# Optimization experiments

Hardware: AMD Instinct MI355X
Metric: run time of the kernel (lower is better)

Reference implementation:

```python
import jax, jax.numpy as jnp
import numpy as np

B, N, D, H, L, C = 64, 64, 64, 256, 64, 2


def setup_inputs() -> dict:
    key = jax.random.key(0)
    ks = iter(jax.random.split(key, 40))

    def p(*shape):
        return (jax.random.normal(next(ks), shape, jnp.float32) / np.sqrt(shape[0])).astype(jnp.float32)

    inp = {
        "x": jax.random.normal(next(ks), (B, N, D), jnp.float32),
        "adj": jax.random.uniform(next(ks), (B, N, N), jnp.float32),
        "condition": jax.random.normal(next(ks), (B, C), jnp.float32),
        # GraphConv layers
        "gc1_W": p(D, H), "gc1_b": jnp.zeros((H,)),
        "gc2_W": p(H, H), "gc2_b": jnp.zeros((H,)),
        "gc3mu_W": p(H, L), "gc3mu_b": jnp.zeros((L,)),
        "gc3lv_W": p(H, L), "gc3lv_b": jnp.zeros((L,)),
        # condition encoder
        "ce_W1": p(C, H), "ce_b1": jnp.zeros((H,)),
        "ce_W2": p(H, H), "ce_b2": jnp.zeros((H,)),
        # decoder
        "dec_W1": p(L + H, H), "dec_b1": jnp.zeros((H,)),
        "dec_W2": p(H, H), "dec_b2": jnp.zeros((H,)),
        "dec_W3": p(H, D), "dec_b3": jnp.zeros((D,)),
        # atom type predictor
        "at_W1": p(D, H), "at_b1": jnp.zeros((H,)),
        "at_W2": p(H, 8), "at_b2": jnp.zeros((8,)),
        # bond predictor
        "bp_W1": p(2 * D + H, H), "bp_b1": jnp.zeros((H,)),
        "bp_W2": p(H, H), "bp_b2": jnp.zeros((H,)),
        "bp_W3": p(H, 4), "bp_b3": jnp.zeros((4,)),
        # rule encoder
        "re_W1": p(D, H), "re_b1": jnp.zeros((H,)),
        "re_W2": p(H, 4), "re_b2": jnp.zeros((4,)),
    }
    return inp


def reference(x, adj, condition,
              gc1_W, gc1_b, gc2_W, gc2_b, gc3mu_W, gc3mu_b, gc3lv_W, gc3lv_b,
              ce_W1, ce_b1, ce_W2, ce_b2,
              dec_W1, dec_b1, dec_W2, dec_b2, dec_W3, dec_b3,
              at_W1, at_b1, at_W2, at_b2,
              bp_W1, bp_b1, bp_W2, bp_b2, bp_W3, bp_b3,
              re_W1, re_b1, re_W2, re_b2):
    relu = jax.nn.relu

    def gc(h, W, b):  # batched GraphConv: adj @ h then linear
        return jnp.einsum('bij,bjd->bid', adj, h) @ W + b

    # encode
    h = relu(gc(x, gc1_W, gc1_b))
    h = relu(gc(h, gc2_W, gc2_b))
    mu = gc(h, gc3mu_W, gc3mu_b)        # [B,N,L]
    logvar = gc(h, gc3lv_W, gc3lv_b)    # [B,N,L]
    z = mu  # eval-mode reparameterize (deterministic)

    # decode: condition encoding broadcast over nodes
    cond = relu(condition @ ce_W1 + ce_b1) @ ce_W2 + ce_b2  # [B,H]
    dec_in = jnp.concatenate([z, jnp.broadcast_to(cond[:, None, :], (z.shape[0], z.shape[1], cond.shape[-1]))], axis=-1)
    f = relu(dec_in @ dec_W1 + dec_b1)
    f = relu(f @ dec_W2 + dec_b2)
    features = jax.nn.sigmoid(f @ dec_W3 + dec_b3)  # [B,N,D]

    type_probs = jax.nn.softmax(relu(features @ at_W1 + at_b1) @ at_W2 + at_b2, axis=-1)  # [B,N,8]
    valence = jax.nn.sigmoid(relu(features @ re_W1 + re_b1) @ re_W2 + re_b2) * 4.0        # [B,N,4]
    atom_features = features * jnp.mean(type_probs, axis=-1, keepdims=True)               # [B,N,D]

    # dense pairwise bond probabilities (vectorized version of the per-pair MLP)
    b, n, d = atom_features.shape
    af_i = jnp.broadcast_to(atom_features[:, :, None, :], (b, n, n, d))
    af_j = jnp.broadcast_to(atom_features[:, None, :, :], (b, n, n, d))
    cnd = jnp.broadcast_to(cond[:, None, None, :], (b, n, n, cond.shape[-1]))
    pair = jnp.concatenate([af_i, af_j, cnd], axis=-1)  # [B,N,N,2D+H]
    g = relu(pair @ bp_W1 + bp_b1)
    g = relu(g @ bp_W2 + bp_b2)
    bond_probs = jax.nn.softmax(g @ bp_W3 + bp_b3, axis=-1)  # [B,N,N,4]

    return (atom_features, bond_probs, valence, mu, logvar)
```

## Files before the change

kernel.cpp:

```cpp
#include <hip/hip_runtime.h>

typedef short short8 __attribute__((ext_vector_type(8)));
typedef float f32x4 __attribute__((ext_vector_type(4)));
typedef unsigned short u16;
typedef unsigned int u32;

__device__ __forceinline__ u16 f2bf(float f) {
  union { float f; u32 u; } x; x.f = f;
  u32 u = x.u;
  u32 r = (u + 0x7FFFu + ((u >> 16) & 1u)) >> 16;
  return (u16)r;
}

__device__ __forceinline__ u32 cvtpk(float lo, float hi) {
  u32 r;
  asm("v_cvt_pk_bf16_f32 %0, %1, %2" : "=v"(r) : "v"(lo), "v"(hi));
  return r;
}

#define OW2T   0
#define OW3TX  65536
#define ODW1A  69632
#define ODW2   86016
#define ODW3   151552
#define OBPA   167936
#define OBPB   184320
#define OREW1  200704
#define OREW2  217088
#define OWMU   221184
#define OWLV   237568

__global__ void __launch_bounds__(512) k_pg(
    const float* __restrict__ cnd, const float* __restrict__ ceW1,
    const float* __restrict__ ceb1, const float* __restrict__ ceW2,
    const float* __restrict__ ceb2, const float* __restrict__ bpW1,
    const float* __restrict__ bpb1, const float* __restrict__ dW1,
    const float* __restrict__ db1, const float* __restrict__ dW2,
    const float* __restrict__ dW3, const float* __restrict__ bpW2,
    const float* __restrict__ bpW3, const float* __restrict__ reW1,
    const float* __restrict__ reW2, const float* __restrict__ gmuW,
    const float* __restrict__ glvW, const float* __restrict__ adj,
    const float* __restrict__ x, const float* __restrict__ gc1W,
    const float* __restrict__ gc1b, float* __restrict__ ctf,
    float* __restrict__ ctv, u16* __restrict__ WB, float* __restrict__ ah1_out) {
  __shared__ char SM[65536];
  int bid = blockIdx.x, t = threadIdx.x;
  if (bid < 126) {
    float* h   = (float*)SM;
    float* c2s = h + 256;
    float* prf = h + 512;
    float* prv = h + 768;
    float (*T)[65] = (float(*)[65])(SM + 4096);
    if (bid < 64) {
      int b = bid;
      if (t < 256) {
        float c0 = cnd[b * 2 + 0], c1 = cnd[b * 2 + 1];
        h[t] = fmaxf(c0 * ceW1[t] + c1 * ceW1[256 + t] + ceb1[t], 0.f);
      }
      __syncthreads();
      int col = t & 255, g = t >> 8;
      {
        float acc = 0.f;
        #pragma unroll 8
        for (int k = g * 128; k < g * 128 + 128; k++) acc += h[k] * ceW2[k * 256 + col];
        if (g) prf[col] = acc;
        __syncthreads();
        if (!g) c2s[col] = acc + prf[col] + ceb2[col];
      }
      __syncthreads();
      float af = 0.f, av = 0.f;
      #pragma unroll 4
      for (int k = g * 128; k < g * 128 + 128; k++) {
        float cv = c2s[k];
        af += cv * bpW1[(128 + k) * 256 + col];
        av += cv * dW1[(64 + k) * 256 + col];
      }
      if (g) { prf[col] = af; prv[col] = av; }
      __syncthreads();
      if (!g) {
        ctf[b * 256 + col] = af + prf[col] + bpb1[col];
        ctv[b * 256 + col] = av + prv[col] + db1[col];
      }
      return;
    }
    int mb = bid - 64;
    if (mb >= 60) {
      if (t < 256) {
        const float* s = (mb == 60) ? reW2 : bpW3;
        u16* d = WB + ((mb == 60) ? OREW2 : OW3TX);
        #pragma unroll
        for (int c = 0; c < 16; c++) {
          float v = (c < 4) ? s[t * 4 + c] : 0.f;
          d[c * 256 + t] = f2bf(v);
        }
      }
      return;
    }
    const float* src; u16* dst; int sld, dld, tr, tc; float sc = 1.f;
    if (mb < 4)       { src = dW1;           dst = WB + ODW1A; sld = 256; dld = 64;  tr = 0;            tc = mb;          }
    else if (mb < 20) { int e = mb - 4;  src = dW2;  dst = WB + ODW2; sld = 256; dld = 256; tr = e >> 2; tc = e & 3; }
    else if (mb < 24) { int e = mb - 20; src = dW3;  dst = WB + ODW3; sld = 64;  dld = 256; tr = e;      tc = 0;     }
    else if (mb < 28) { int e = mb - 24; src = bpW1; dst = WB + OBPA; sld = 256; dld = 64;  tr = 0;      tc = e; sc = 0.125f; }
    else if (mb < 32) { int e = mb - 28; src = bpW1 + 64 * 256; dst = WB + OBPB; sld = 256; dld = 64; tr = 0; tc = e; sc = 0.125f; }
    else if (mb < 36) { int e = mb - 32; src = reW1; dst = WB + OREW1; sld = 256; dld = 64; tr = 0;      tc = e;     }
    else if (mb < 40) { int e = mb - 36; src = gmuW; dst = WB + OWMU; sld = 64;  dld = 256; tr = e;      tc = 0;     }
    else if (mb < 44) { int e = mb - 40; src = glvW; dst = WB + OWLV; sld = 64;  dld = 256; tr = e;      tc = 0;     }
    else              { int e = mb - 44; src = bpW2; dst = WB + OW2T; sld = 256; dld = 256; tr = e >> 2; tc = e & 3; }
    int rl = t >> 6, cl = t & 63;
    #pragma unroll
    for (int it = 0; it < 8; it++) {
      int r = it * 8 + rl;
      T[r][cl] = src[(tr * 64 + r) * sld + tc * 64 + cl] * sc;
    }
    __syncthreads();
    #pragma unroll
    for (int it = 0; it < 8; it++) {
      int c2_ = it * 8 + rl;
      dst[(tc * 64 + c2_) * dld + tr * 64 + cl] = f2bf(T[cl][c2_]);
    }
    return;
  }
  int e2 = bid - 126;
  int cg = e2 & 3, b = e2 >> 2;
  float* adj_s = (float*)SM;
  float* x_s   = adj_s + 4096;
  float* ax_s  = adj_s + 8192;
  float* h_s   = adj_s + 12288;
  const float* A = adj + b * 4096;
  const float* X = x + b * 4096;
  for (int e = t; e < 4096; e += 512) { adj_s[e] = A[e]; x_s[e] = X[e]; }
  __syncthreads();
  int c = t & 63, rg = t >> 6;
  {
    float acc[8];
    #pragma unroll
    for (int m = 0; m < 8; m++) acc[m] = 0.f;
    #pragma unroll 4
    for (int j4 = 0; j4 < 16; j4++) {
      float xv0 = x_s[(j4 * 4 + 0) * 64 + c];
      float xv1 = x_s[(j4 * 4 + 1) * 64 + c];
      float xv2 = x_s[(j4 * 4 + 2) * 64 + c];
      float xv3 = x_s[(j4 * 4 + 3) * 64 + c];
      #pragma unroll
      for (int m = 0; m < 8; m++) {
        float4 a4 = *(const float4*)&adj_s[(m * 8 + rg) * 64 + j4 * 4];
        acc[m] += a4.x * xv0 + a4.y * xv1 + a4.z * xv2 + a4.w * xv3;
      }
    }
    #pragma unroll
    for (int m = 0; m < 8; m++) ax_s[(m * 8 + rg) * 64 + c] = acc[m];
  }
  __syncthreads();
  {
    float bv = gc1b[cg * 64 + c];
    float acc[8];
    #pragma unroll
    for (int m = 0; m < 8; m++) acc[m] = bv;
    #pragma unroll 4
    for (int k4 = 0; k4 < 16; k4++) {
      float w0 = gc1W[(k4 * 4 + 0) * 256 + cg * 64 + c];
      float w1 = gc1W[(k4 * 4 + 1) * 256 + cg * 64 + c];
      float w2 = gc1W[(k4 * 4 + 2) * 256 + cg * 64 + c];
      float w3 = gc1W[(k4 * 4 + 3) * 256 + cg * 64 + c];
      #pragma unroll
      for (int m = 0; m < 8; m++) {
        float4 a4 = *(const float4*)&ax_s[(m * 8 + rg) * 64 + k4 * 4];
        acc[m] += a4.x * w0 + a4.y * w1 + a4.z * w2 + a4.w * w3;
      }
    }
    #pragma unroll
    for (int m = 0; m < 8; m++) h_s[(m * 8 + rg) * 64 + c] = fmaxf(acc[m], 0.f);
  }
  __syncthreads();
  {
    float acc[8];
    #pragma unroll
    for (int m = 0; m < 8; m++) acc[m] = 0.f;
    #pragma unroll 4
    for (int j4 = 0; j4 < 16; j4++) {
      float h0 = h_s[(j4 * 4 + 0) * 64 + c];
      float h1 = h_s[(j4 * 4 + 1) * 64 + c];
      float h2 = h_s[(j4 * 4 + 2) * 64 + c];
      float h3 = h_s[(j4 * 4 + 3) * 64 + c];
      #pragma unroll
      for (int m = 0; m < 8; m++) {
        float4 a4 = *(const float4*)&adj_s[(m * 8 + rg) * 64 + j4 * 4];
        acc[m] += a4.x * h0 + a4.y * h1 + a4.z * h2 + a4.w * h3;
      }
    }
    float* O = ah1_out + b * 64 * 256 + cg * 64;
    #pragma unroll
    for (int m = 0; m < 8; m++) O[(m * 8 + rg) * 256 + c] = acc[m];
  }
}

__global__ void __launch_bounds__(512) k_linadj(
    const float* __restrict__ adj, const float* __restrict__ in,
    const float* __restrict__ W, const float* __restrict__ bias,
    float* __restrict__ out) {
  __shared__ float adj_s[64 * 64];
  __shared__ float in_s[32 * 256];
  __shared__ float h_s[64 * 64];
  int cg = blockIdx.x, b = blockIdx.y, t = threadIdx.x;
  const float* A = adj + b * 4096;
  for (int e = t; e < 4096; e += 512) adj_s[e] = A[e];
  int c = t & 63, rg = t >> 6;
  float bv = bias[cg * 64 + c];
  #pragma unroll
  for (int half = 0; half < 2; half++) {
    if (half) __syncthreads();
    const float* I = in + (b * 64 + half * 32) * 256;
    for (int e = t; e < 32 * 256; e += 512) in_s[e] = I[e];
    __syncthreads();
    float acc[4];
    #pragma unroll
    for (int m = 0; m < 4; m++) acc[m] = bv;
    #pragma unroll 4
    for (int k4 = 0; k4 < 64; k4++) {
      float w0 = W[(k4 * 4 + 0) * 256 + cg * 64 + c];
      float w1 = W[(k4 * 4 + 1) * 256 + cg * 64 + c];
      float w2 = W[(k4 * 4 + 2) * 256 + cg * 64 + c];
      float w3 = W[(k4 * 4 + 3) * 256 + cg * 64 + c];
      #pragma unroll
      for (int m = 0; m < 4; m++) {
        float4 i4 = *(const float4*)&in_s[(m * 8 + rg) * 256 + k4 * 4];
        acc[m] += i4.x * w0 + i4.y * w1 + i4.z * w2 + i4.w * w3;
      }
    }
    #pragma unroll
    for (int m = 0; m < 4; m++)
      h_s[(half * 32 + m * 8 + rg) * 64 + c] = fmaxf(acc[m], 0.f);
  }
  __syncthreads();
  {
    float acc[8];
    #pragma unroll
    for (int m = 0; m < 8; m++) acc[m] = 0.f;
    #pragma unroll 4
    for (int j4 = 0; j4 < 16; j4++) {
      float h0 = h_s[(j4 * 4 + 0) * 64 + c];
      float h1 = h_s[(j4 * 4 + 1) * 64 + c];
      float h2 = h_s[(j4 * 4 + 2) * 64 + c];
      float h3 = h_s[(j4 * 4 + 3) * 64 + c];
      #pragma unroll
      for (int m = 0; m < 8; m++) {
        float4 a4 = *(const float4*)&adj_s[(m * 8 + rg) * 64 + j4 * 4];
        acc[m] += a4.x * h0 + a4.y * h1 + a4.z * h2 + a4.w * h3;
      }
    }
    float* O = out + b * 64 * 256 + cg * 64;
    #pragma unroll
    for (int m = 0; m < 8; m++) O[(m * 8 + rg) * 256 + c] = acc[m];
  }
}

template <int KK, int WU, int WV, bool UG, bool VG, int ULEN, int VLEN>
__device__ __forceinline__ void mmrun(const u16* __restrict__ Up, int Uoff,
                                      const u16* __restrict__ Vp, int Voff,
                                      const char* lds, int ut0, int vt0, int lr, int lk,
                                      f32x4 (&acc)[WU][WV]) {
  #pragma unroll
  for (int kk = 0; kk < KK; kk++) {
    short8 uf[WU], vf[WV];
    #pragma unroll
    for (int i = 0; i < WU; i++) {
      int row = (ut0 + i) * 16 + lr;
      if constexpr (UG) {
        uf[i] = *(const short8*)(Up + row * ULEN + kk * 32 + lk * 8);
      } else {
        int byt = Uoff + row * (ULEN * 2) + kk * 64 + lk * 16;
        byt ^= (row & 7) << 4;
        uf[i] = *(const short8*)(lds + byt);
      }
    }
    #pragma unroll
    for (int j = 0; j < WV; j++) {
      int row = (vt0 + j) * 16 + lr;
      if constexpr (VG) {
        vf[j] = *(const short8*)(Vp + row * VLEN + kk * 32 + lk * 8);
      } else {
        int byt = Voff + row * (VLEN * 2) + kk * 64 + lk * 16;
        byt ^= (row & 7) << 4;
        vf[j] = *(const short8*)(lds + byt);
      }
    }
    #pragma unroll
    for (int i = 0; i < WU; i++)
      #pragma unroll
      for (int j = 0; j < WV; j++)
        acc[i][j] = __builtin_amdgcn_mfma_f32_16x16x32_bf16(uf[i], vf[j], acc[i][j], 0, 0, 0);
  }
}

__device__ __forceinline__ void st64(char* lds, int off, int rowlen, int crow, int ccol0,
                                     float a0, float a1, float a2, float a3) {
  uint2 pk; pk.x = cvtpk(a0, a1); pk.y = cvtpk(a2, a3);
  int byt = off + crow * (rowlen * 2) + ccol0 * 2;
  byt ^= (crow & 7) << 4;
  *(uint2*)(lds + byt) = pk;
}

template <int WU, int WV>
__device__ __forceinline__ void zacc(f32x4 (&acc)[WU][WV]) {
  #pragma unroll
  for (int i = 0; i < WU; i++)
    #pragma unroll
    for (int j = 0; j < WV; j++) acc[i][j] = (f32x4){0.f, 0.f, 0.f, 0.f};
}

__global__ void __launch_bounds__(1024) k_chain2(
    const u16* __restrict__ WB, const float* __restrict__ ah2_g,
    const float* __restrict__ ctv, const float* __restrict__ ctf,
    const float* __restrict__ gmub, const float* __restrict__ glvb,
    const float* __restrict__ db2, const float* __restrict__ db3,
    const float* __restrict__ reb1, const float* __restrict__ reb2,
    float* __restrict__ mu_out, float* __restrict__ lv_out,
    float* __restrict__ af_out, float* __restrict__ val_out,
    float* __restrict__ P, float* __restrict__ Q) {
  __shared__ char L[65536];
  constexpr int S2 = 0, S3 = 32768;
  int b = blockIdx.x, t = threadIdx.x;
  int w = t >> 6, lane = t & 63, lr = lane & 15, lk = lane >> 4;

  {
    int r = t >> 4, cb = (t & 15) * 16;
    #pragma unroll
    for (int q = 0; q < 4; q++) {
      float4 v = *(const float4*)(ah2_g + ((b * 64 + r) * 256 + cb + q * 4));
      st64(L, S2, 256, r, cb + q * 4, v.x, v.y, v.z, v.w);
    }
  }
  __syncthreads();
  {
    f32x4 a[2][1]; zacc(a);
    int sel = w >> 3, wq = w & 7;
    int ut0 = (wq & 1) * 2, vt = wq >> 1;
    const u16* Up = WB + (sel ? OWLV : OWMU);
    mmrun<8, 2, 1, true, false, 256, 256>(Up, 0, WB, S2, L, ut0, vt, lr, lk, a);
    int crow = vt * 16 + lr;
    const float* bb = sel ? glvb : gmub;
    float* gout = sel ? lv_out : mu_out;
    #pragma unroll
    for (int i = 0; i < 2; i++) {
      int cc = (ut0 + i) * 16 + lk * 4;
      float4 bv = *(const float4*)(bb + cc);
      float o0 = a[i][0][0] + bv.x, o1 = a[i][0][1] + bv.y;
      float o2 = a[i][0][2] + bv.z, o3 = a[i][0][3] + bv.w;
      *(float4*)(gout + ((b * 64 + crow) * 64 + cc)) = make_float4(o0, o1, o2, o3);
      if (sel == 0) st64(L, S3, 64, crow, cc, o0, o1, o2, o3);
    }
  }
  __syncthreads();
  {
    f32x4 a[2][2]; zacc(a);
    int ut0 = (w & 7) * 2, vt0 = (w >> 3) * 2;
    mmrun<2, 2, 2, true, false, 64, 64>(WB + ODW1A, 0, WB, S3, L, ut0, vt0, lr, lk, a);
    #pragma unroll
    for (int j = 0; j < 2; j++) {
      int crow = (vt0 + j) * 16 + lr;
      #pragma unroll
      for (int i = 0; i < 2; i++) {
        int cc = (ut0 + i) * 16 + lk * 4;
        float4 cv = *(const float4*)(ctv + b * 256 + cc);
        st64(L, S2, 256, crow, cc, fmaxf(a[i][j][0] + cv.x, 0.f), fmaxf(a[i][j][1] + cv.y, 0.f),
             fmaxf(a[i][j][2] + cv.z, 0.f), fmaxf(a[i][j][3] + cv.w, 0.f));
      }
    }
  }
  __syncthreads();
  {
    f32x4 a[2][2]; zacc(a);
    int ut0 = (w & 7) * 2, vt0 = (w >> 3) * 2;
    mmrun<8, 2, 2, true, false, 256, 256>(WB + ODW2, 0, WB, S2, L, ut0, vt0, lr, lk, a);
    #pragma unroll
    for (int j = 0; j < 2; j++) {
      int crow = (vt0 + j) * 16 + lr;
      #pragma unroll
      for (int i = 0; i < 2; i++) {
        int cc = (ut0 + i) * 16 + lk * 4;
        float4 bv = *(const float4*)(db2 + cc);
        st64(L, S3, 256, crow, cc, fmaxf(a[i][j][0] + bv.x, 0.f), fmaxf(a[i][j][1] + bv.y, 0.f),
             fmaxf(a[i][j][2] + bv.z, 0.f), fmaxf(a[i][j][3] + bv.w, 0.f));
      }
    }
  }
  __syncthreads();
  {
    f32x4 a[1][1]; zacc(a);
    int ut = w & 3, vt = w >> 2;
    mmrun<8, 1, 1, true, false, 256, 256>(WB + ODW3, 0, WB, S3, L, ut, vt, lr, lk, a);
    int crow = vt * 16 + lr, cc = ut * 16 + lk * 4;
    float4 bv = *(const float4*)(db3 + cc);
    float s0 = 1.f / (1.f + expf(-(a[0][0][0] + bv.x)));
    float s1 = 1.f / (1.f + expf(-(a[0][0][1] + bv.y)));
    float s2 = 1.f / (1.f + expf(-(a[0][0][2] + bv.z)));
    float s3 = 1.f / (1.f + expf(-(a[0][0][3] + bv.w)));
    *(float4*)(af_out + ((b * 64 + crow) * 64 + cc)) =
        make_float4(s0 * 0.125f, s1 * 0.125f, s2 * 0.125f, s3 * 0.125f);
    st64(L, S2, 64, crow, cc, s0, s1, s2, s3);
  }
  __syncthreads();
  {
    f32x4 a[2][4]; zacc(a);
    int ut0 = (w & 7) * 2;
    int sel = w >> 3;
    const u16* Up = WB + (sel ? OBPB : OBPA);
    mmrun<2, 2, 4, true, false, 64, 64>(Up, 0, WB, S2, L, ut0, 0, lr, lk, a);
    float* out = sel ? Q : P;
    #pragma unroll
    for (int i = 0; i < 2; i++) {
      int cc = (ut0 + i) * 16 + lk * 4;
      float4 cv = make_float4(0.f, 0.f, 0.f, 0.f);
      if (sel == 0) cv = *(const float4*)(ctf + b * 256 + cc);
      #pragma unroll
      for (int j = 0; j < 4; j++) {
        int crow = j * 16 + lr;
        *(float4*)(out + ((b * 64 + crow) * 256 + cc)) =
            make_float4(a[i][j][0] + cv.x, a[i][j][1] + cv.y, a[i][j][2] + cv.z, a[i][j][3] + cv.w);
      }
    }
  }
  {
    f32x4 a[2][2]; zacc(a);
    int ut0 = (w & 7) * 2, vt0 = (w >> 3) * 2;
    mmrun<2, 2, 2, true, false, 64, 64>(WB + OREW1, 0, WB, S2, L, ut0, vt0, lr, lk, a);
    #pragma unroll
    for (int j = 0; j < 2; j++) {
      int crow = (vt0 + j) * 16 + lr;
      #pragma unroll
      for (int i = 0; i < 2; i++) {
        int cc = (ut0 + i) * 16 + lk * 4;
        float4 bv = *(const float4*)(reb1 + cc);
        st64(L, S3, 256, crow, cc, fmaxf(a[i][j][0] + bv.x, 0.f), fmaxf(a[i][j][1] + bv.y, 0.f),
             fmaxf(a[i][j][2] + bv.z, 0.f), fmaxf(a[i][j][3] + bv.w, 0.f));
      }
    }
  }
  __syncthreads();
  if (w < 4) {
    f32x4 a[1][1]; zacc(a);
    mmrun<8, 1, 1, true, false, 256, 256>(WB + OREW2, 0, WB, S3, L, 0, w, lr, lk, a);
    if (lk == 0) {
      float4 rb = *(const float4*)reb2;
      float v0 = 4.f / (1.f + expf(-(a[0][0][0] + rb.x)));
      float v1 = 4.f / (1.f + expf(-(a[0][0][1] + rb.y)));
      float v2 = 4.f / (1.f + expf(-(a[0][0][2] + rb.z)));
      float v3 = 4.f / (1.f + expf(-(a[0][0][3] + rb.w)));
      *(float4*)(val_out + (b * 64 + w * 16 + lr) * 4) = make_float4(v0, v1, v2, v3);
    }
  }
}

__global__ void __launch_bounds__(512, 4) k_bond(
    const float* __restrict__ P, const float* __restrict__ Q,
    const u16* __restrict__ W2T, const float* __restrict__ b2,
    const u16* __restrict__ W3Tx, const float* __restrict__ b3,
    float* __restrict__ bp_out) {
  __shared__ u16 G[2 * 64 * 256];
  int flat = blockIdx.x;
  int xcd = flat & 7, rest = flat >> 3;
  int b = xcd * 8 + (rest >> 5);
  int i0 = (rest & 31) * 2;
  int t = threadIdx.x;
  int lane = t & 63, w = t >> 6;
  int lr = lane & 15, lk = lane >> 4;

  {
    int colg = t & 63, rq = t >> 6;
    const float* Pb = P + (b * 64 + i0) * 256 + colg * 4;
    float4 p0 = *(const float4*)(Pb);
    float4 p1 = *(const float4*)(Pb + 256);
    const float* Qb = Q + b * 64 * 256;
    #pragma unroll
    for (int r = rq * 8; r < rq * 8 + 8; r++) {
      float4 q4 = *(const float4*)(Qb + r * 256 + colg * 4);
      int byt = (r * 512 + colg * 8) ^ ((r & 7) << 4);
      uint2 pk0, pk1;
      pk0.x = cvtpk(fmaxf(p0.x + q4.x, 0.f), fmaxf(p0.y + q4.y, 0.f));
      pk0.y = cvtpk(fmaxf(p0.z + q4.z, 0.f), fmaxf(p0.w + q4.w, 0.f));
      pk1.x = cvtpk(fmaxf(p1.x + q4.x, 0.f), fmaxf(p1.y + q4.y, 0.f));
      pk1.y = cvtpk(fmaxf(p1.z + q4.z, 0.f), fmaxf(p1.w + q4.w, 0.f));
      *(uint2*)((char*)G + byt) = pk0;
      *(uint2*)((char*)G + 32768 + byt) = pk1;
    }
  }
  __syncthreads();

  f32x4 acc[2][2][4];
  #pragma unroll
  for (int tl = 0; tl < 2; tl++)
    #pragma unroll
    for (int ni = 0; ni < 2; ni++)
      #pragma unroll
      for (int mi = 0; mi < 4; mi++) acc[tl][ni][mi] = (f32x4){0.f, 0.f, 0.f, 0.f};

  const u16* Wl = W2T + (w * 32 + lr) * 256 + lk * 8;
  short8 bwc0 = *(const short8*)(Wl);
  short8 bwc1 = *(const short8*)(Wl + 16 * 256);
  for (int kk = 0; kk < 8; kk++) {
    int kn = (kk + 1) & 7;
    short8 bwn0 = *(const short8*)(Wl + kn * 32);
    short8 bwn1 = *(const short8*)(Wl + 16 * 256 + kn * 32);
    __builtin_amdgcn_s_setprio(1);
    #pragma unroll
    for (int mi = 0; mi < 4; mi++) {
      int row = mi * 16 + lr;
      int byt = (row * 512 + kk * 64 + lk * 16) ^ ((row & 7) << 4);
      short8 a0 = *(const short8*)((const char*)G + byt);
      short8 a1 = *(const short8*)((const char*)G + 32768 + byt);
      acc[0][0][mi] = __builtin_amdgcn_mfma_f32_16x16x32_bf16(bwc0, a0, acc[0][0][mi], 0, 0, 0);
      acc[1][0][mi] = __builtin_amdgcn_mfma_f32_16x16x32_bf16(bwc0, a1, acc[1][0][mi], 0, 0, 0);
      acc[0][1][mi] = __builtin_amdgcn_mfma_f32_16x16x32_bf16(bwc1, a0, acc[0][1][mi], 0, 0, 0);
      acc[1][1][mi] = __builtin_amdgcn_mfma_f32_16x16x32_bf16(bwc1, a1, acc[1][1][mi], 0, 0, 0);
    }
    __builtin_amdgcn_s_setprio(0);
    bwc0 = bwn0;
    bwc1 = bwn1;
  }
  __syncthreads();

  #pragma unroll
  for (int tl = 0; tl < 2; tl++)
    #pragma unroll
    for (int ni = 0; ni < 2; ni++) {
      int col0 = w * 32 + ni * 16 + lk * 4;
      float4 bb = *(const float4*)(b2 + col0);
      #pragma unroll
      for (int mi = 0; mi < 4; mi++) {
        int grow = mi * 16 + lr;
        uint2 pk;
        pk.x = cvtpk(fmaxf(acc[tl][ni][mi][0] + bb.x, 0.f), fmaxf(acc[tl][ni][mi][1] + bb.y, 0.f));
        pk.y = cvtpk(fmaxf(acc[tl][ni][mi][2] + bb.z, 0.f), fmaxf(acc[tl][ni][mi][3] + bb.w, 0.f));
        int byt = ((grow * 512 + col0 * 2) ^ ((grow & 7) << 4)) + tl * 32768;
        *(uint2*)((char*)G + byt) = pk;
      }
    }
  __syncthreads();

  f32x4 acc2[2][4];
  #pragma unroll
  for (int tl = 0; tl < 2; tl++)
    #pragma unroll
    for (int mi = 0; mi < 4; mi++) acc2[tl][mi] = (f32x4){0.f, 0.f, 0.f, 0.f};
  {
    short8 bw2 = *(const short8*)(W3Tx + lr * 256 + w * 32 + lk * 8);
    #pragma unroll
    for (int tl = 0; tl < 2; tl++)
      #pragma unroll
      for (int mi = 0; mi < 4; mi++) {
        int row = mi * 16 + lr;
        int byt = ((row * 512 + (w * 32 + lk * 8) * 2) ^ ((row & 7) << 4)) + tl * 32768;
        short8 a = *(const short8*)((const char*)G + byt);
        acc2[tl][mi] = __builtin_amdgcn_mfma_f32_16x16x32_bf16(a, bw2, acc2[tl][mi], 0, 0, 0);
      }
  }
  __syncthreads();
  float* pf = (float*)G;
  if (lr < 4) {
    #pragma unroll
    for (int tl = 0; tl < 2; tl++)
      #pragma unroll
      for (int mi = 0; mi < 4; mi++)
        #pragma unroll
        for (int rg = 0; rg < 4; rg++) {
          int row = mi * 16 + lk * 4 + rg;
          pf[tl * 8192 + (w * 64 + row) * 4 + lr] = acc2[tl][mi][rg];
        }
  }
  __syncthreads();

  {
    int tl = t >> 8, idx = t & 255;
    int r = idx >> 2, c = idx & 3;
    float lv = b3[c];
    #pragma unroll
    for (int wq = 0; wq < 8; wq++) lv += pf[tl * 8192 + (wq * 64 + r) * 4 + c];
    float m = fmaxf(lv, __shfl_xor(lv, 1));
    m = fmaxf(m, __shfl_xor(m, 2));
    float e = expf(lv - m);
    float s = e + __shfl_xor(e, 1);
    s += __shfl_xor(s, 2);
    bp_out[((b * 64 + i0 + tl) * 64 + r) * 4 + c] = e / s;
  }
}

extern "C" void kernel_launch(void* const* d_in, const int* in_sizes, int n_in,
                              void* d_out, int out_size, void* d_ws, size_t ws_size,
                              hipStream_t stream) {
  const float* x    = (const float*)d_in[0];
  const float* adj  = (const float*)d_in[1];
  const float* cnd  = (const float*)d_in[2];
  const float* gc1W = (const float*)d_in[3];
  const float* gc1b = (const float*)d_in[4];
  const float* gc2W = (const float*)d_in[5];
  const float* gc2b = (const float*)d_in[6];
  const float* gmuW = (const float*)d_in[7];
  const float* gmub = (const float*)d_in[8];
  const float* glvW = (const float*)d_in[9];
  const float* glvb = (const float*)d_in[10];
  const float* ceW1 = (const float*)d_in[11];
  const float* ceb1 = (const float*)d_in[12];
  const float* ceW2 = (const float*)d_in[13];
  const float* ceb2 = (const float*)d_in[14];
  const float* dW1  = (const float*)d_in[15];
  const float* db1  = (const float*)d_in[16];
  const float* dW2  = (const float*)d_in[17];
  const float* db2  = (const float*)d_in[18];
  const float* dW3  = (const float*)d_in[19];
  const float* db3  = (const float*)d_in[20];
  const float* bpW1 = (const float*)d_in[25];
  const float* bpb1 = (const float*)d_in[26];
  const float* bpW2 = (const float*)d_in[27];
  const float* bpb2 = (const float*)d_in[28];
  const float* bpW3 = (const float*)d_in[29];
  const float* bpb3 = (const float*)d_in[30];
  const float* reW1 = (const float*)d_in[31];
  const float* reb1 = (const float*)d_in[32];
  const float* reW2 = (const float*)d_in[33];
  const float* reb2 = (const float*)d_in[34];

  float* out = (float*)d_out;
  float* af_out  = out;
  float* bp_out  = out + 262144;
  float* val_out = out + 1310720;
  float* mu_out  = out + 1327104;
  float* lv_out  = out + 1589248;

  float* ws   = (float*)d_ws;
  float* ctf  = ws;
  float* ctv  = ws + 16384;
  float* buf1 = ws + 49152;
  float* buf2 = buf1 + 1048576;
  float* buf3 = buf2 + 1048576;
  u16*   WB   = (u16*)(buf3 + 1048576);

  k_pg<<<382, 512, 0, stream>>>(cnd, ceW1, ceb1, ceW2, ceb2, bpW1, bpb1, dW1, db1,
                                dW2, dW3, bpW2, bpW3, reW1, reW2, gmuW, glvW,
                                adj, x, gc1W, gc1b, ctf, ctv, WB, buf3);
  k_linadj<<<dim3(4, 64), 512, 0, stream>>>(adj, buf3, gc2W, gc2b, buf1);
  k_chain2<<<64, 1024, 0, stream>>>(WB, buf1, ctv, ctf, gmub, glvb, db2, db3,
                                    reb1, reb2, mu_out, lv_out, af_out, val_out,
                                    buf2, buf3);
  k_bond<<<2048, 512, 0, stream>>>(buf2, buf3, WB + OW2T, bpb2, WB + OW3TX, bpb3, bp_out);
}
```

Before: 140.8 us.

## Split k_chain2 per batch into four 16-row blocks for more parallelism

The per-node MLP chain kernel moves from 64 blocks of 1024 threads (one graph per block) to 256 blocks of 512 threads, each handling 16 rows of one graph. Every stage's work decomposition is reworked so each wave covers 16 rows and a column tile, and LDS shrinks from 64KB to 16KB. The aim is to fill more CUs on the GPU, which a 64-block launch leaves mostly idle. The cost is that each block re-reads the full weight matrices, so weight traffic per row goes up.

```diff
diff --git a/kernel.cpp b/kernel.cpp
--- a/kernel.cpp
+++ b/kernel.cpp
@@ -308,7 +308,7 @@
     for (int j = 0; j < WV; j++) acc[i][j] = (f32x4){0.f, 0.f, 0.f, 0.f};
 }
 
-__global__ void __launch_bounds__(1024) k_chain2(
+__global__ void __launch_bounds__(512) k_chain2(
     const u16* __restrict__ WB, const float* __restrict__ ah2_g,
     const float* __restrict__ ctv, const float* __restrict__ ctf,
     const float* __restrict__ gmub, const float* __restrict__ glvb,
@@ -317,136 +317,117 @@
     float* __restrict__ mu_out, float* __restrict__ lv_out,
     float* __restrict__ af_out, float* __restrict__ val_out,
     float* __restrict__ P, float* __restrict__ Q) {
-  __shared__ char L[65536];
-  constexpr int S2 = 0, S3 = 32768;
-  int b = blockIdx.x, t = threadIdx.x;
+  __shared__ char L[16384];
+  constexpr int S2 = 0, S3 = 8192;
+  int rb = blockIdx.x;
+  int b = rb >> 2, r0 = (rb & 3) << 4;
+  int gr0 = b * 64 + r0;
+  int t = threadIdx.x;
   int w = t >> 6, lane = t & 63, lr = lane & 15, lk = lane >> 4;
 
   {
-    int r = t >> 4, cb = (t & 15) * 16;
-    #pragma unroll
-    for (int q = 0; q < 4; q++) {
-      float4 v = *(const float4*)(ah2_g + ((b * 64 + r) * 256 + cb + q * 4));
-      st64(L, S2, 256, r, cb + q * 4, v.x, v.y, v.z, v.w);
-    }
-  }
-  __syncthreads();
-  {
-    f32x4 a[2][1]; zacc(a);
-    int sel = w >> 3, wq = w & 7;
-    int ut0 = (wq & 1) * 2, vt = wq >> 1;
+    int r = t >> 5, c0 = (t & 31) * 8;
+    const float* src = ah2_g + (gr0 + r) * 256 + c0;
+    float4 v0 = *(const float4*)(src);
+    float4 v1 = *(const float4*)(src + 4);
+    st64(L, S2, 256, r, c0, v0.x, v0.y, v0.z, v0.w);
+    st64(L, S2, 256, r, c0 + 4, v1.x, v1.y, v1.z, v1.w);
+  }
+  __syncthreads();
+  {
+    f32x4 a[1][1]; zacc(a);
+    int sel = w >> 2, ut = w & 3;
     const u16* Up = WB + (sel ? OWLV : OWMU);
-    mmrun<8, 2, 1, true, false, 256, 256>(Up, 0, WB, S2, L, ut0, vt, lr, lk, a);
-    int crow = vt * 16 + lr;
+    mmrun<8, 1, 1, true, false, 256, 256>(Up + ut * 16 * 256, 0, WB, S2, L, 0, 0, lr, lk, a);
     const float* bb = sel ? glvb : gmub;
     float* gout = sel ? lv_out : mu_out;
+    int cc = ut * 16 + lk * 4;
+    float4 bv = *(const float4*)(bb + cc);
+    float o0 = a[0][0][0] + bv.x, o1 = a[0][0][1] + bv.y;
+    float o2 = a[0][0][2] + bv.z, o3 = a[0][0][3] + bv.w;
+    *(float4*)(gout + (gr0 + lr) * 64 + cc) = make_float4(o0, o1, o2, o3);
+    if (sel == 0) st64(L, S3, 64, lr, cc, o0, o1, o2, o3);
+  }
+  __syncthreads();
+  {
+    f32x4 a[2][1]; zacc(a);
+    int ut0 = w * 2;
+    mmrun<2, 2, 1, true, false, 64, 64>(WB + ODW1A, 0, WB, S3, L, ut0, 0, lr, lk, a);
     #pragma unroll
     for (int i = 0; i < 2; i++) {
       int cc = (ut0 + i) * 16 + lk * 4;
-      float4 bv = *(const float4*)(bb + cc);
-      float o0 = a[i][0][0] + bv.x, o1 = a[i][0][1] + bv.y;
-      float o2 = a[i][0][2] + bv.z, o3 = a[i][0][3] + bv.w;
-      *(float4*)(gout + ((b * 64 + crow) * 64 + cc)) = make_float4(o0, o1, o2, o3);
-      if (sel == 0) st64(L, S3, 64, crow, cc, o0, o1, o2, o3);
-    }
-  }
-  __syncthreads();
-  {
-    f32x4 a[2][2]; zacc(a);
-    int ut0 = (w & 7) * 2, vt0 = (w >> 3) * 2;
-    mmrun<2, 2, 2, true, false, 64, 64>(WB + ODW1A, 0, WB, S3, L, ut0, vt0, lr, lk, a);
-    #pragma unroll
-    for (int j = 0; j < 2; j++) {
-      int crow = (vt0 + j) * 16 + lr;
-      #pragma unroll
-      for (int i = 0; i < 2; i++) {
-        int cc = (ut0 + i) * 16 + lk * 4;
-        float4 cv = *(const float4*)(ctv + b * 256 + cc);
-        st64(L, S2, 256, crow, cc, fmaxf(a[i][j][0] + cv.x, 0.f), fmaxf(a[i][j][1] + cv.y, 0.f),
-             fmaxf(a[i][j][2] + cv.z, 0.f), fmaxf(a[i][j][3] + cv.w, 0.f));
-      }
-    }
-  }
-  __syncthreads();
-  {
-    f32x4 a[2][2]; zacc(a);
-    int ut0 = (w & 7) * 2, vt0 = (w >> 3) * 2;
-    mmrun<8, 2, 2, true, false, 256, 256>(WB + ODW2, 0, WB, S2, L, ut0, vt0, lr, lk, a);
-    #pragma unroll
-    for (int j = 0; j < 2; j++) {
-      int crow = (vt0 + j) * 16 + lr;
-      #pragma unroll
-      for (int i = 0; i < 2; i++) {
-        int cc = (ut0 + i) * 16 + lk * 4;
-        float4 bv = *(const float4*)(db2 + cc);
-        st64(L, S3, 256, crow, cc, fmaxf(a[i][j][0] + bv.x, 0.f), fmaxf(a[i][j][1] + bv.y, 0.f),
-             fmaxf(a[i][j][2] + bv.z, 0.f), fmaxf(a[i][j][3] + bv.w, 0.f));
-      }
-    }
-  }
-  __syncthreads();
-  {
+      float4 cv = *(const float4*)(ctv + b * 256 + cc);
+      st64(L, S2, 256, lr, cc, fmaxf(a[i][0][0] + cv.x, 0.f), fmaxf(a[i][0][1] + cv.y, 0.f),
+           fmaxf(a[i][0][2] + cv.z, 0.f), fmaxf(a[i][0][3] + cv.w, 0.f));
+    }
+  }
+  __syncthreads();
+  {
+    f32x4 a[2][1]; zacc(a);
+    int ut0 = w * 2;
+    mmrun<8, 2, 1, true, false, 256, 256>(WB + ODW2, 0, WB, S2, L, ut0, 0, lr, lk, a);
+    #pragma unroll
+    for (int i = 0; i < 2; i++) {
+      int cc = (ut0 + i) * 16 + lk * 4;
+      float4 bv = *(const float4*)(db2 + cc);
+      st64(L, S3, 256, lr, cc, fmaxf(a[i][0][0] + bv.x, 0.f), fmaxf(a[i][0][1] + bv.y, 0.f),
+           fmaxf(a[i][0][2] + bv.z, 0.f), fmaxf(a[i][0][3] + bv.w, 0.f));
+    }
+  }
+  __syncthreads();
+  if (w < 4) {
     f32x4 a[1][1]; zacc(a);
-    int ut = w & 3, vt = w >> 2;
-    mmrun<8, 1, 1, true, false, 256, 256>(WB + ODW3, 0, WB, S3, L, ut, vt, lr, lk, a);
-    int crow = vt * 16 + lr, cc = ut * 16 + lk * 4;
+    int ut = w;
+    mmrun<8, 1, 1, true, false, 256, 256>(WB + ODW3 + ut * 16 * 256, 0, WB, S3, L, 0, 0, lr, lk, a);
+    int cc = ut * 16 + lk * 4;
     float4 bv = *(const float4*)(db3 + cc);
     float s0 = 1.f / (1.f + expf(-(a[0][0][0] + bv.x)));
     float s1 = 1.f / (1.f + expf(-(a[0][0][1] + bv.y)));
     float s2 = 1.f / (1.f + expf(-(a[0][0][2] + bv.z)));
     float s3 = 1.f / (1.f + expf(-(a[0][0][3] + bv.w)));
-    *(float4*)(af_out + ((b * 64 + crow) * 64 + cc)) =
+    *(float4*)(af_out + (gr0 + lr) * 64 + cc) =
         make_float4(s0 * 0.125f, s1 * 0.125f, s2 * 0.125f, s3 * 0.125f);
-    st64(L, S2, 64, crow, cc, s0, s1, s2, s3);
-  }
-  __syncthreads();
-  {
-    f32x4 a[2][4]; zacc(a);
-    int ut0 = (w & 7) * 2;
-    int sel = w >> 3;
+    st64(L, S2, 64, lr, cc, s0, s1, s2, s3);
+  }
+  __syncthreads();
+  {
+    f32x4 a[4][1]; zacc(a);
+    int sel = w >> 2, ut0 = (w & 3) * 4;
     const u16* Up = WB + (sel ? OBPB : OBPA);
-    mmrun<2, 2, 4, true, false, 64, 64>(Up, 0, WB, S2, L, ut0, 0, lr, lk, a);
+    mmrun<2, 4, 1, true, false, 64, 64>(Up, 0, WB, S2, L, ut0, 0, lr, lk, a);
     float* out = sel ? Q : P;
     #pragma unroll
-    for (int i = 0; i < 2; i++) {
+    for (int i = 0; i < 4; i++) {
       int cc = (ut0 + i) * 16 + lk * 4;
       float4 cv = make_float4(0.f, 0.f, 0.f, 0.f);
       if (sel == 0) cv = *(const float4*)(ctf + b * 256 + cc);
-      #pragma unroll
-      for (int j = 0; j < 4; j++) {
-        int crow = j * 16 + lr;
-        *(float4*)(out + ((b * 64 + crow) * 256 + cc)) =
-            make_float4(a[i][j][0] + cv.x, a[i][j][1] + cv.y, a[i][j][2] + cv.z, a[i][j][3] + cv.w);
-      }
-    }
-  }
-  {
-    f32x4 a[2][2]; zacc(a);
-    int ut0 = (w & 7) * 2, vt0 = (w >> 3) * 2;
-    mmrun<2, 2, 2, true, false, 64, 64>(WB + OREW1, 0, WB, S2, L, ut0, vt0, lr, lk, a);
-    #pragma unroll
-    for (int j = 0; j < 2; j++) {
-      int crow = (vt0 + j) * 16 + lr;
-      #pragma unroll
-      for (int i = 0; i < 2; i++) {
-        int cc = (ut0 + i) * 16 + lk * 4;
-        float4 bv = *(const float4*)(reb1 + cc);
-        st64(L, S3, 256, crow, cc, fmaxf(a[i][j][0] + bv.x, 0.f), fmaxf(a[i][j][1] + bv.y, 0.f),
-             fmaxf(a[i][j][2] + bv.z, 0.f), fmaxf(a[i][j][3] + bv.w, 0.f));
-      }
-    }
-  }
-  __syncthreads();
-  if (w < 4) {
+      *(float4*)(out + (gr0 + lr) * 256 + cc) =
+          make_float4(a[i][0][0] + cv.x, a[i][0][1] + cv.y, a[i][0][2] + cv.z, a[i][0][3] + cv.w);
+    }
+  }
+  {
+    f32x4 a[2][1]; zacc(a);
+    int ut0 = w * 2;
+    mmrun<2, 2, 1, true, false, 64, 64>(WB + OREW1, 0, WB, S2, L, ut0, 0, lr, lk, a);
+    #pragma unroll
+    for (int i = 0; i < 2; i++) {
+      int cc = (ut0 + i) * 16 + lk * 4;
+      float4 bv = *(const float4*)(reb1 + cc);
+      st64(L, S3, 256, lr, cc, fmaxf(a[i][0][0] + bv.x, 0.f), fmaxf(a[i][0][1] + bv.y, 0.f),
+           fmaxf(a[i][0][2] + bv.z, 0.f), fmaxf(a[i][0][3] + bv.w, 0.f));
+    }
+  }
+  __syncthreads();
+  if (w == 0) {
     f32x4 a[1][1]; zacc(a);
-    mmrun<8, 1, 1, true, false, 256, 256>(WB + OREW2, 0, WB, S3, L, 0, w, lr, lk, a);
+    mmrun<8, 1, 1, true, false, 256, 256>(WB + OREW2, 0, WB, S3, L, 0, 0, lr, lk, a);
     if (lk == 0) {
       float4 rb = *(const float4*)reb2;
       float v0 = 4.f / (1.f + expf(-(a[0][0][0] + rb.x)));
       float v1 = 4.f / (1.f + expf(-(a[0][0][1] + rb.y)));
       float v2 = 4.f / (1.f + expf(-(a[0][0][2] + rb.z)));
       float v3 = 4.f / (1.f + expf(-(a[0][0][3] + rb.w)));
-      *(float4*)(val_out + (b * 64 + w * 16 + lr) * 4) = make_float4(v0, v1, v2, v3);
+      *(float4*)(val_out + (gr0 + lr) * 4) = make_float4(v0, v1, v2, v3);
     }
   }
 }
@@ -638,7 +619,7 @@
                                 dW2, dW3, bpW2, bpW3, reW1, reW2, gmuW, glvW,
                                 adj, x, gc1W, gc1b, ctf, ctv, WB, buf3);
   k_linadj<<<dim3(4, 64), 512, 0, stream>>>(adj, buf3, gc2W, gc2b, buf1);
-  k_chain2<<<64, 1024, 0, stream>>>(WB, buf1, ctv, ctf, gmub, glvb, db2, db3,
+  k_chain2<<<256, 512, 0, stream>>>(WB, buf1, ctv, ctf, gmub, glvb, db2, db3,
                                     reb1, reb2, mu_out, lv_out, af_out, val_out,
                                     buf2, buf3);
   k_bond<<<2048, 512, 0, stream>>>(buf2, buf3, WB + OW2T, bpb2, WB + OW3TX, bpb3, bp_out);
```

After: 125.0 us. -11.2%, faster.
